# Optimization experiments

Measured on AMD Instinct MI355X. Metric: run time of the kernel, lower is better.

The kernel has to match this reference:

```python
import jax, jax.numpy as jnp
import numpy as np

N = 100_000   # nodes
E = 1_600_000 # edges
C = 64        # in = hidden = out channels
H = 8         # heads
D = C // H    # head_dim = 8
R = 4         # relations
L = 2         # layers


def setup_inputs() -> dict:
    key = jax.random.key(0)
    ks = jax.random.split(key, 10)
    sc = 1.0 / np.sqrt(C)  # xavier-ish scale
    return {
        "x": jax.random.normal(ks[0], (N, C), jnp.float32),
        "edge_index": jax.random.randint(ks[1], (2, E), 0, N),
        "edge_type": jax.random.randint(ks[2], (E,), 0, R),
        "W_Q": jax.random.normal(ks[3], (L, R, H, C, D), jnp.float32) * sc,
        "W_K": jax.random.normal(ks[4], (L, R, H, C, D), jnp.float32) * sc,
        "W_V": jax.random.normal(ks[5], (L, R, H, C, D), jnp.float32) * sc,
        "W_concat": jax.random.normal(ks[6], (L, R, H * D, C), jnp.float32) * sc,
        "sem_w": jax.random.normal(ks[7], (L, C), jnp.float32) * sc,
        "sem_b": jnp.zeros((L,), jnp.float32),
        "W_self": jax.random.normal(ks[8], (L, C, C), jnp.float32) * sc,
        "ln_g": jnp.ones((L, C), jnp.float32),
        "ln_b": jnp.zeros((L, C), jnp.float32),
    }


def _layer(x, src, dst, edge_type, WQ, WK, WV, Wcat, sw, sb, Ws, g, b):
    inv_sqrt_d = 1.0 / np.sqrt(D)
    rel_msgs = []
    for r in range(R):  # small fixed relation loop
        mask = (edge_type == r).astype(x.dtype)             # (E,)
        Q = jnp.einsum('nc,hcd->nhd', x, WQ[r])             # (N,H,D)
        K = jnp.einsum('nc,hcd->nhd', x, WK[r])
        V = jnp.einsum('nc,hcd->nhd', x, WV[r])
        # edge-wise QK energy, leaky_relu(0.01), scatter-add into dst node
        energy = jnp.einsum('ehd,ehd->eh', Q[dst], K[src]) * inv_sqrt_d
        energy = jax.nn.leaky_relu(energy)                  # (E,H)
        alpha_n = jax.ops.segment_sum(energy * mask[:, None], dst,
                                      num_segments=N)       # (N,H)
        alpha = jax.nn.softmax(alpha_n, axis=0)             # softmax over nodes
        w = alpha[dst] * mask[:, None]                      # (E,H)
        m = jax.ops.segment_sum(w[:, :, None] * V[src], dst,
                                num_segments=N)             # (N,H,D)
        rel_msgs.append(m.reshape(N, H * D) @ Wcat[r])      # (N,C)
    stacked = jnp.stack(rel_msgs)                           # (R,N,C)
    beta = jax.nn.softmax(stacked @ sw + sb, axis=0)        # (R,N) semantic attn
    agg = jnp.einsum('rn,rnc->nc', beta, stacked)           # (N,C)
    y = x + jax.nn.gelu(x @ Ws + agg, approximate=False)
    mu = y.mean(-1, keepdims=True)
    var = y.var(-1, keepdims=True)
    return (y - mu) / jnp.sqrt(var + 1e-5) * g + b


def reference(x, edge_index, edge_type, W_Q, W_K, W_V, W_concat,
              sem_w, sem_b, W_self, ln_g, ln_b):
    src, dst = edge_index[0], edge_index[1]  # PyG source_to_target: j=row0, i=row1
    for l in range(L):
        x = _layer(x, src, dst, edge_type, W_Q[l], W_K[l], W_V[l], W_concat[l],
                   sem_w[l], sem_b[l], W_self[l], ln_g[l], ln_b[l])
        # inter-layer dropout omitted (inference / eval mode)
    return x
```

## Files before the change

### kernel.cpp

```cpp
#include <hip/hip_runtime.h>
#include <hip/hip_bf16.h>

#define NN 100000
#define EE 1600000
#define RRR 4
#define HHH 8
#define NT 400000
#define GG 782
#define SHIFT 9
#define NBLK 512
#define CHUNK 3125
#define BMAX 2560

typedef unsigned int u32;
typedef unsigned short u16;
typedef __attribute__((ext_vector_type(8))) short bf16x8;
typedef __attribute__((ext_vector_type(4))) float f32x4;

static constexpr size_t OFF_KV   = 0;
static constexpr size_t OFF_Q    = 102400000;
static constexpr size_t OFF_S    = 153600000;
static constexpr size_t OFF_SELF = 204800000;
static constexpr size_t OFF_AL   = 217600000;
static constexpr size_t OFF_PW   = 230400000;
static constexpr size_t OFF_PART = 230700000;
static constexpr size_t OFF_FIN  = 230710000;
static constexpr size_t OFF_CW   = 230720000;
static constexpr size_t OFF_LG   = 230730000;
static constexpr size_t OFF_ROWP = 232400000;
static constexpr size_t OFF_EDG  = 234100000;
static constexpr size_t OFF_BSTORE = OFF_S;
static constexpr size_t OFF_HIST   = OFF_S + 8000000;
static constexpr size_t OFF_OFFA   = OFF_S + 16000000;
static constexpr size_t OFF_BASE   = OFF_S + 24000000;

__device__ inline u16 f2bf(float f){
  union { __hip_bfloat16 h; u16 u; } cv; cv.h = __float2bfloat16(f); return cv.u;
}
__device__ inline float bf2f(u16 u){ return __uint_as_float(((u32)u) << 16); }

__global__ __launch_bounds__(256) void k_histA(const int* __restrict__ dst, const int* __restrict__ typ,
                                               u32* __restrict__ Hist){
  __shared__ u32 h[GG];
  int b = blockIdx.x, t = threadIdx.x;
  for (int g = t; g < GG; g += 256) h[g] = 0u;
  __syncthreads();
  int e0 = b * CHUNK;
  for (int e = e0 + t; e < e0 + CHUNK; e += 256){
    int seg = typ[e] * NN + dst[e];
    atomicAdd(&h[seg >> SHIFT], 1u);
  }
  __syncthreads();
  for (int g = t; g < GG; g += 256) Hist[(size_t)b * GG + g] = h[g];
}

__global__ __launch_bounds__(1024) void k_base(const u32* __restrict__ Hist, u32* __restrict__ Base,
                                               u32* __restrict__ rowp){
  __shared__ u32 tot[GG];
  int t = threadIdx.x;
  if (t < GG){
    u32 s = 0;
    for (int b = 0; b < NBLK; b++) s += Hist[(size_t)b * GG + t];
    tot[t] = s;
  }
  __syncthreads();
  if (t == 0){
    u32 acc = 0;
    for (int g = 0; g < GG; g++){ u32 c = tot[g]; Base[g] = acc; acc += c; }
    Base[GG] = acc;
    rowp[NT] = EE;
  }
}

__global__ __launch_bounds__(512) void k_off(const u32* __restrict__ Hist, const u32* __restrict__ Base,
                                             u32* __restrict__ Off){
  __shared__ u32 v[NBLK];
  int g = blockIdx.x, t = threadIdx.x;
  v[t] = Hist[(size_t)t * GG + g];
  __syncthreads();
  if (t == 0){
    u32 acc = Base[g];
    for (int b = 0; b < NBLK; b++){ u32 c = v[b]; v[b] = acc; acc += c; }
  }
  __syncthreads();
  Off[(size_t)g * NBLK + t] = v[t];
}

__global__ __launch_bounds__(256) void k_fill(const int* __restrict__ src, const int* __restrict__ dst,
                                              const int* __restrict__ typ, const u32* __restrict__ Off,
                                              u32* __restrict__ bstore){
  __shared__ u32 cur[GG];
  int b = blockIdx.x, t = threadIdx.x;
  for (int g = t; g < GG; g += 256) cur[g] = Off[(size_t)g * NBLK + b];
  __syncthreads();
  int e0 = b * CHUNK;
  for (int e = e0 + t; e < e0 + CHUNK; e += 256){
    int seg = typ[e] * NN + dst[e];
    u32 pos = atomicAdd(&cur[seg >> SHIFT], 1u);
    bstore[pos] = ((u32)(seg & 511) << 17) | (u32)src[e];
  }
}

__global__ __launch_bounds__(256) void k_sortD(const u32* __restrict__ bstore, const u32* __restrict__ Base,
                                               u32* __restrict__ rowp, u32* __restrict__ edges){
  __shared__ u32 ent[BMAX];
  __shared__ u32 binc[512], bexc[512];
  int g = blockIdx.x, t = threadIdx.x;
  u32 base = Base[g];
  u32 cnt = Base[g + 1] - base;
  if (cnt > (u32)BMAX) cnt = (u32)BMAX;
  for (int i = t; i < 512; i += 256) binc[i] = 0u;
  __syncthreads();
  for (u32 i = t; i < cnt; i += 256){
    u32 v = bstore[base + i];
    ent[i] = v;
    atomicAdd(&binc[v >> 17], 1u);
  }
  __syncthreads();
  if (t == 0){
    u32 acc = 0;
    #pragma unroll 8
    for (int s = 0; s < 512; s++){ u32 c = binc[s]; bexc[s] = acc; binc[s] = acc; acc += c; }
  }
  __syncthreads();
  for (int s = t; s < 512; s += 256){
    int seg = g * 512 + s;
    if (seg < NT) rowp[seg] = base + bexc[s];
  }
  __syncthreads();
  for (u32 i = t; i < cnt; i += 256){
    u32 v = ent[i];
    u32 p = atomicAdd(&binc[v >> 17], 1u);
    edges[base + p] = v & 0x1FFFFu;
  }
}

__global__ __launch_bounds__(256) void k_repackbf(const float* __restrict__ WQ, const float* __restrict__ WK,
                                                  const float* __restrict__ WV, const float* __restrict__ Wcat,
                                                  const float* __restrict__ Wself, u16* __restrict__ pwB){
  int t = blockIdx.x * 256 + threadIdx.x;
  if (t >= 2 * 17 * 4096) return;
  int l = t / (17 * 4096), rem = t % (17 * 4096);
  int mat = rem >> 12, idx = rem & 4095;
  int out = idx >> 6, c = idx & 63;
  float v;
  if (mat < 12){
    int kind = mat >> 2, r = mat & 3;
    int h = out >> 3, d = out & 7;
    const float* Wsrc = (kind == 0) ? WQ : (kind == 1) ? WK : WV;
    v = Wsrc[((((l * RRR + r) * HHH + h) * 64) + c) * 8 + d];
  } else if (mat == 12){
    v = Wself[(l * 64 + c) * 64 + out];
  } else {
    int r = mat - 13;
    v = Wcat[(((l * RRR + r) * 64) + c) * 64 + out];
  }
  pwB[t] = f2bf(v);
}

__global__ __launch_bounds__(512) void k_cw(const float* __restrict__ Wcat, const float* __restrict__ semw,
                                            float* __restrict__ cw){
  int t = threadIdx.x;
  int l = t >> 8, r = (t >> 6) & 3, k = t & 63;
  const float* wp = Wcat + (((size_t)(l * RRR + r) * 64) + k) * 64;
  const float* sp = semw + l * 64;
  float s = 0.f;
  #pragma unroll 8
  for (int c = 0; c < 64; c++) s += wp[c] * sp[c];
  cw[t] = s;
}


__global__ __launch_bounds__(256) void k_qkvself(const float* __restrict__ x, const u16* __restrict__ pwL,
                                                 u16* __restrict__ QAll, u16* __restrict__ selfb,
                                                 u32* __restrict__ kvpAll){
  __shared__ u16 xa[64][72];
  int t = threadIdx.x;
  int n0 = blockIdx.x * 64;
  {
    int row = t >> 2, c0 = (t & 3) * 16;
    int n = n0 + row;
    float4 v0 = {}, v1 = {}, v2 = {}, v3 = {};
    if (n < NN){
      const float4* xp = (const float4*)(x + (size_t)n * 64 + c0);
      v0 = xp[0]; v1 = xp[1]; v2 = xp[2]; v3 = xp[3];
    }
    ushort4* dp = (ushort4*)&xa[row][c0];
    dp[0] = make_ushort4(f2bf(v0.x), f2bf(v0.y), f2bf(v0.z), f2bf(v0.w));
    dp[1] = make_ushort4(f2bf(v1.x), f2bf(v1.y), f2bf(v1.z), f2bf(v1.w));
    dp[2] = make_ushort4(f2bf(v2.x), f2bf(v2.y), f2bf(v2.z), f2bf(v2.w));
    dp[3] = make_ushort4(f2bf(v3.x), f2bf(v3.y), f2bf(v3.z), f2bf(v3.w));
  }
  __syncthreads();
  int w = t >> 6, lane = t & 63;
  int ra = w * 16 + (lane & 15);
  int kg = (lane >> 4) * 8;
  int cb = lane & 15;
  int rb = (lane >> 4) * 4;
  bf16x8 a0 = *(const bf16x8*)&xa[ra][kg];
  bf16x8 a1 = *(const bf16x8*)&xa[ra][32 + kg];
  f32x4 z = {0.f, 0.f, 0.f, 0.f};
  #pragma unroll
  for (int m = 0; m < 5; m++){
    const u16* wp = pwL + (size_t)((m < 4) ? m : 12) * 4096;
    f32x4 acc[4] = {z, z, z, z};
    #pragma unroll
    for (int t4 = 0; t4 < 4; t4++){
      bf16x8 b0 = *(const bf16x8*)(wp + (t4 * 16 + cb) * 64 + kg);
      bf16x8 b1 = *(const bf16x8*)(wp + (t4 * 16 + cb) * 64 + 32 + kg);
      acc[t4] = __builtin_amdgcn_mfma_f32_16x16x32_bf16(a0, b0, acc[t4], 0, 0, 0);
      acc[t4] = __builtin_amdgcn_mfma_f32_16x16x32_bf16(a1, b1, acc[t4], 0, 0, 0);
    }
    u16* op = (m < 4) ? (QAll + (size_t)m * NN * 64) : selfb;
    #pragma unroll
    for (int t4 = 0; t4 < 4; t4++){
      #pragma unroll
      for (int i2 = 0; i2 < 4; i2++){
        int n = n0 + w * 16 + rb + i2;
        if (n < NN) op[(size_t)n * 64 + t4 * 16 + cb] = f2bf(acc[t4][i2]);
      }
    }
  }
  #pragma unroll
  for (int r = 0; r < 4; r++){
    const u16* wk = pwL + (size_t)(4 + r) * 4096;
    const u16* wv = pwL + (size_t)(8 + r) * 4096;
    f32x4 ak[4] = {z, z, z, z};
    f32x4 av[4] = {z, z, z, z};
    #pragma unroll
    for (int t4 = 0; t4 < 4; t4++){
      bf16x8 bk0 = *(const bf16x8*)(wk + (t4 * 16 + cb) * 64 + kg);
      bf16x8 bk1 = *(const bf16x8*)(wk + (t4 * 16 + cb) * 64 + 32 + kg);
      bf16x8 bv0 = *(const bf16x8*)(wv + (t4 * 16 + cb) * 64 + kg);
      bf16x8 bv1 = *(const bf16x8*)(wv + (t4 * 16 + cb) * 64 + 32 + kg);
      ak[t4] = __builtin_amdgcn_mfma_f32_16x16x32_bf16(a0, bk0, ak[t4], 0, 0, 0);
      ak[t4] = __builtin_amdgcn_mfma_f32_16x16x32_bf16(a1, bk1, ak[t4], 0, 0, 0);
      av[t4] = __builtin_amdgcn_mfma_f32_16x16x32_bf16(a0, bv0, av[t4], 0, 0, 0);
      av[t4] = __builtin_amdgcn_mfma_f32_16x16x32_bf16(a1, bv1, av[t4], 0, 0, 0);
    }
    u32* kp = kvpAll + (size_t)r * NN * 64;
    #pragma unroll
    for (int t4 = 0; t4 < 4; t4++){
      #pragma unroll
      for (int i2 = 0; i2 < 4; i2++){
        int n = n0 + w * 16 + rb + i2;
        if (n < NN) kp[(size_t)n * 64 + t4 * 16 + cb] = (u32)f2bf(ak[t4][i2]) | ((u32)f2bf(av[t4][i2]) << 16);
      }
    }
  }
}

__global__ __launch_bounds__(256) void k_gather4(const u32* __restrict__ edges, const u32* __restrict__ rowp,
                                                 const u32* __restrict__ kvpAll, const u16* __restrict__ QAll,
                                                 u16* __restrict__ Sb, float* __restrict__ alphaB){
  int wid = threadIdx.x >> 6, lane = threadIdx.x & 63;
  int qt = lane >> 4;
  int i  = lane & 15;
  int n = blockIdx.x * 4 + wid;
  const float isd = 0.35355339059327373f;
  #pragma unroll
  for (int r = 0; r < 4; r++){
    const u32* kvp = kvpAll + (size_t)r * NN * 64;
    ushort4 qv = *(const ushort4*)&QAll[((size_t)r * NN + n) * 64 + 4 * i];
    float q0 = bf2f(qv.x), q1 = bf2f(qv.y), q2 = bf2f(qv.z), q3 = bf2f(qv.w);
    u32 beg = rowp[(size_t)r * NN + n], end = rowp[(size_t)r * NN + n + 1];
    float sx = 0.f, sy = 0.f, sz = 0.f, sw = 0.f, aa = 0.f;
    for (u32 base = beg; base < end; base += 64){
      u32 cnt = (end - base < 64u) ? (end - base) : 64u;
      u32 eidx = (base + (u32)lane < end) ? edges[base + lane] : 0u;
      for (u32 j = 0; j < cnt; j += 4){
        u32 jj = j + (u32)qt;
        float mk = (jj < cnt) ? 1.f : 0.f;
        u32 js = (jj < cnt) ? jj : (cnt - 1);
        int s = __shfl((int)eidx, (int)js);
        uint4 w = *(const uint4*)&kvp[(size_t)s * 64 + 4 * i];
        float p = q0 * bf2f((u16)(w.x & 0xFFFFu)) + q1 * bf2f((u16)(w.y & 0xFFFFu))
                + q2 * bf2f((u16)(w.z & 0xFFFFu)) + q3 * bf2f((u16)(w.w & 0xFFFFu));
        p += __shfl_xor(p, 1);
        float e = p * isd;
        e = (e > 0.f) ? e : 0.01f * e;
        aa += e * mk;
        sx += bf2f((u16)(w.x >> 16)) * mk;
        sy += bf2f((u16)(w.y >> 16)) * mk;
        sz += bf2f((u16)(w.z >> 16)) * mk;
        sw += bf2f((u16)(w.w >> 16)) * mk;
      }
    }
    sx += __shfl_xor(sx, 16); sx += __shfl_xor(sx, 32);
    sy += __shfl_xor(sy, 16); sy += __shfl_xor(sy, 32);
    sz += __shfl_xor(sz, 16); sz += __shfl_xor(sz, 32);
    sw += __shfl_xor(sw, 16); sw += __shfl_xor(sw, 32);
    aa += __shfl_xor(aa, 16); aa += __shfl_xor(aa, 32);
    if (qt == 0){
      ushort4 o; o.x = f2bf(sx); o.y = f2bf(sy); o.z = f2bf(sz); o.w = f2bf(sw);
      *(ushort4*)&Sb[((size_t)r * NN + n) * 64 + 4 * i] = o;
      if ((i & 1) == 0) alphaB[((size_t)r * NN + n) * 8 + (i >> 1)] = aa;
    }
  }
}

__global__ __launch_bounds__(256) void k_stats1(const float* __restrict__ alpha, float2* __restrict__ part){
  int r = blockIdx.y;
  int chunk = blockIdx.x;
  const int per = (NN + 31) / 32;
  int nbeg = chunk * per;
  int nend = nbeg + per; if (nend > NN) nend = NN;
  int t = threadIdx.x;
  int h = t & 7;
  int g = t >> 3;
  float m = -1e30f, s = 0.f;
  for (int n = nbeg + g; n < nend; n += 32){
    float a = alpha[((size_t)r * NN + n) * 8 + h];
    if (a > m){ s *= expf(m - a); m = a; }
    s += expf(a - m);
  }
  __shared__ float sm[256], ss[256];
  sm[t] = m; ss[t] = s; __syncthreads();
  for (int off = 128; off >= 8; off >>= 1){
    if (t < off){
      float m2 = sm[t + off], s2 = ss[t + off];
      float M = fmaxf(sm[t], m2);
      ss[t] = ss[t] * expf(sm[t] - M) + s2 * expf(m2 - M);
      sm[t] = M;
    }
    __syncthreads();
  }
  if (t < 8) part[(r * 8 + t) * 32 + chunk] = make_float2(sm[t], ss[t]);
}

__global__ void k_stats2(const float2* __restrict__ part, float2* __restrict__ fin){
  int col = threadIdx.x;
  if (col < 32){
    float M = -1e30f, S = 0.f;
    for (int i = 0; i < 32; i++){
      float2 p = part[col * 32 + i];
      float Mn = fmaxf(M, p.x);
      S = S * expf(M - Mn) + p.y * expf(p.x - Mn);
      M = Mn;
    }
    fin[col] = make_float2(M, 1.f / S);
  }
}

__global__ __launch_bounds__(256) void k_msg(const u16* __restrict__ S, const float* __restrict__ alpha,
                                             const float2* __restrict__ fin, const u16* __restrict__ pwCat,
                                             const float* __restrict__ cwL, float* __restrict__ lgbuf,
                                             u16* __restrict__ stacked){
  __shared__ u16 xa[64][72];
  __shared__ u16 wt[64][72];
  int r = blockIdx.y;
  int t = threadIdx.x;
  int n0 = blockIdx.x * 64;
  {
    int row = t >> 2, c0 = (t & 3) * 16;
    int n = n0 + row;
    int na = (n < NN) ? n : (NN - 1);
    int h0 = c0 >> 3;
    float2 f0 = fin[r * 8 + h0];
    float2 f1 = fin[r * 8 + h0 + 1];
    float a0 = alpha[((size_t)r * NN + na) * 8 + h0];
    float a1 = alpha[((size_t)r * NN + na) * 8 + h0 + 1];
    float w0 = expf(a0 - f0.x) * f0.y;
    float w1 = expf(a1 - f1.x) * f1.y;
    const u32* sp = (const u32*)(S + ((size_t)r * NN + na) * 64 + c0);
    const float* cwr = cwL + r * 64;
    float lgp = 0.f;
    #pragma unroll
    for (int jj = 0; jj < 8; jj++){
      u32 bts = sp[jj];
      float wm = (jj < 4) ? w0 : w1;
      float mv0 = bf2f((u16)(bts & 0xFFFFu)) * wm;
      float mv1 = bf2f((u16)(bts >> 16)) * wm;
      lgp += mv0 * cwr[c0 + jj * 2] + mv1 * cwr[c0 + jj * 2 + 1];
      ushort2 o;
      o.x = f2bf(mv0);
      o.y = f2bf(mv1);
      *(ushort2*)&xa[row][c0 + jj * 2] = o;
    }
    lgp += __shfl_xor(lgp, 1);
    lgp += __shfl_xor(lgp, 2);
    if ((t & 3) == 0 && n < NN) lgbuf[(size_t)r * NN + n] = lgp;
  }
  {
    const u32* p0 = (const u32*)(pwCat + (size_t)r * 4096);
    for (int idx = t; idx < 2048; idx += 256){
      int out = idx >> 5, cc = idx & 31;
      *(u32*)&wt[out][cc * 2] = p0[idx];
    }
  }
  __syncthreads();
  int w = t >> 6, lane = t & 63;
  int ra = w * 16 + (lane & 15);
  int kg = (lane >> 4) * 8;
  int cb = lane & 15;
  int rb = (lane >> 4) * 4;
  bf16x8 a0 = *(const bf16x8*)&xa[ra][kg];
  bf16x8 a1 = *(const bf16x8*)&xa[ra][32 + kg];
  f32x4 z = {0.f, 0.f, 0.f, 0.f};
  f32x4 acc[4] = {z, z, z, z};
  #pragma unroll
  for (int t4 = 0; t4 < 4; t4++){
    bf16x8 b0 = *(const bf16x8*)&wt[t4 * 16 + cb][kg];
    bf16x8 b1 = *(const bf16x8*)&wt[t4 * 16 + cb][32 + kg];
    acc[t4] = __builtin_amdgcn_mfma_f32_16x16x32_bf16(a0, b0, acc[t4], 0, 0, 0);
    acc[t4] = __builtin_amdgcn_mfma_f32_16x16x32_bf16(a1, b1, acc[t4], 0, 0, 0);
  }
  #pragma unroll
  for (int t4 = 0; t4 < 4; t4++){
    #pragma unroll
    for (int i = 0; i < 4; i++){
      int n = n0 + w * 16 + rb + i;
      if (n < NN) stacked[((size_t)r * NN + n) * 64 + t4 * 16 + cb] = f2bf(acc[t4][i]);
    }
  }
}

__global__ __launch_bounds__(256) void k_final(const u16* __restrict__ stacked, const u16* __restrict__ selfb,
                                               const float* __restrict__ xin, const float* __restrict__ lgbuf,
                                               const float* __restrict__ lng, const float* __restrict__ lnb,
                                               float* __restrict__ xout){
  int t = threadIdx.x;
  int wid = t >> 6, lane = t & 63;
  int n = blockIdx.x * 4 + wid;
  float st[4];
  #pragma unroll
  for (int r = 0; r < 4; r++) st[r] = bf2f(stacked[((size_t)r * NN + n) * 64 + lane]);
  float lg0 = lgbuf[n];
  float lg1 = lgbuf[(size_t)NN + n];
  float lg2 = lgbuf[(size_t)2 * NN + n];
  float lg3 = lgbuf[(size_t)3 * NN + n];
  float mx = fmaxf(fmaxf(lg0, lg1), fmaxf(lg2, lg3));
  float e0 = expf(lg0 - mx), e1 = expf(lg1 - mx), e2 = expf(lg2 - mx), e3 = expf(lg3 - mx);
  float inv = 1.f / (e0 + e1 + e2 + e3);
  float agg = (e0 * st[0] + e1 * st[1] + e2 * st[2] + e3 * st[3]) * inv;
  float pre = bf2f(selfb[(size_t)n * 64 + lane]) + agg;
  float ge = 0.5f * pre * (1.f + erff(pre * 0.70710678118654752f));
  float y = xin[(size_t)n * 64 + lane] + ge;
  float mu = y;
  #pragma unroll
  for (int o = 1; o < 64; o <<= 1) mu += __shfl_xor(mu, o);
  mu *= (1.f / 64.f);
  float d = y - mu;
  float vv = d * d;
  #pragma unroll
  for (int o = 1; o < 64; o <<= 1) vv += __shfl_xor(vv, o);
  vv *= (1.f / 64.f);
  xout[(size_t)n * 64 + lane] = d * rsqrtf(vv + 1e-5f) * lng[lane] + lnb[lane];
}

extern "C" void kernel_launch(void* const* d_in, const int* in_sizes, int n_in,
                              void* d_out, int out_size, void* d_ws, size_t ws_size,
                              hipStream_t stream){
  const float* x0    = (const float*)d_in[0];
  const int*   eidx  = (const int*)d_in[1];
  const int*   etyp  = (const int*)d_in[2];
  const float* WQ    = (const float*)d_in[3];
  const float* WK    = (const float*)d_in[4];
  const float* WV    = (const float*)d_in[5];
  const float* Wcat  = (const float*)d_in[6];
  const float* semw  = (const float*)d_in[7];
  const float* semb  = (const float*)d_in[8];
  const float* Wself = (const float*)d_in[9];
  const float* lng   = (const float*)d_in[10];
  const float* lnb   = (const float*)d_in[11];
  float* out = (float*)d_out;
  char* ws = (char*)d_ws;

  const int* srcArr = eidx;
  const int* dstArr = eidx + EE;

  u32*  kvpAll   = (u32*)(ws + OFF_KV);
  u16*  Qb       = (u16*)(ws + OFF_Q);
  u16*  stackedB = (u16*)(ws + OFF_Q);
  u16*  Sb       = (u16*)(ws + OFF_S);
  u16*  selfb    = (u16*)(ws + OFF_SELF);
  float* alphaB  = (float*)(ws + OFF_AL);
  u16*  pwB      = (u16*)(ws + OFF_PW);
  float2* part   = (float2*)(ws + OFF_PART);
  float2* fin    = (float2*)(ws + OFF_FIN);
  float* cw      = (float*)(ws + OFF_CW);
  float* lgbuf   = (float*)(ws + OFF_LG);
  u32* rowp   = (u32*)(ws + OFF_ROWP);
  u32* edges  = (u32*)(ws + OFF_EDG);
  u32* bstore = (u32*)(ws + OFF_BSTORE);
  u32* Hist   = (u32*)(ws + OFF_HIST);
  u32* Off    = (u32*)(ws + OFF_OFFA);
  u32* Base   = (u32*)(ws + OFF_BASE);

  k_histA<<<NBLK, 256, 0, stream>>>(dstArr, etyp, Hist);
  k_base<<<1, 1024, 0, stream>>>(Hist, Base, rowp);
  k_off<<<GG, 512, 0, stream>>>(Hist, Base, Off);
  k_fill<<<NBLK, 256, 0, stream>>>(srcArr, dstArr, etyp, Off, bstore);
  k_sortD<<<GG, 256, 0, stream>>>(bstore, Base, rowp, edges);
  k_repackbf<<<(2 * 17 * 4096 + 255) / 256, 256, 0, stream>>>(WQ, WK, WV, Wcat, Wself, pwB);
  k_cw<<<1, 512, 0, stream>>>(Wcat, semw, cw);

  for (int l = 0; l < 2; l++){
    const float* xcur = (l == 0) ? x0 : out;
    const u16* pwL = pwB + (size_t)l * 17 * 4096;
    k_qkvself<<<1563, 256, 0, stream>>>(xcur, pwL, Qb, selfb, kvpAll);
    k_gather4<<<NN / 4, 256, 0, stream>>>(edges, rowp, kvpAll, Qb, Sb, alphaB);
    k_stats1<<<dim3(32, 4), 256, 0, stream>>>(alphaB, part);
    k_stats2<<<1, 64, 0, stream>>>(part, fin);
    k_msg<<<dim3(1563, 4), 256, 0, stream>>>(Sb, alphaB, fin, pwL + (size_t)13 * 4096,
                                             cw + l * 256, lgbuf, stackedB);
    k_final<<<NN / 4, 256, 0, stream>>>(stackedB, selfb, xcur, lgbuf,
                                        lng + l * 64, lnb + l * 64, out);
  }
  (void)in_sizes; (void)n_in; (void)out_size; (void)ws_size;
  (void)semb;
}
```

Measured before the change: 725.2 us.

## Fuse message projection, semantic attention, self-GEMM and LayerNorm into one kernel

Merges k_msg (per-relation Wcat projection) and k_final (semantic softmax, GELU, residual, LayerNorm) into one kernel that handles all four relations per 64-node tile. The semantic weights are computed in shared memory and applied to the MFMA results in registers. The x@W_self GEMM moves out of k_qkvself into the fused kernel. This avoids writing and re-reading the bf16 stacked buffer, selfb and lgbuf and removes one launch per layer. The cost is much larger shared memory per block (about 46KB), which may lower occupancy, and Wcat is now read from global memory instead of staged in LDS.

```diff
diff --git a/kernel.cpp b/kernel.cpp
--- a/kernel.cpp
+++ b/kernel.cpp
@@ -20,13 +20,11 @@
 static constexpr size_t OFF_KV   = 0;
 static constexpr size_t OFF_Q    = 102400000;
 static constexpr size_t OFF_S    = 153600000;
-static constexpr size_t OFF_SELF = 204800000;
 static constexpr size_t OFF_AL   = 217600000;
 static constexpr size_t OFF_PW   = 230400000;
 static constexpr size_t OFF_PART = 230700000;
 static constexpr size_t OFF_FIN  = 230710000;
 static constexpr size_t OFF_CW   = 230720000;
-static constexpr size_t OFF_LG   = 230730000;
 static constexpr size_t OFF_ROWP = 232400000;
 static constexpr size_t OFF_EDG  = 234100000;
 static constexpr size_t OFF_BSTORE = OFF_S;
@@ -172,8 +170,7 @@
 
 
 __global__ __launch_bounds__(256) void k_qkvself(const float* __restrict__ x, const u16* __restrict__ pwL,
-                                                 u16* __restrict__ QAll, u16* __restrict__ selfb,
-                                                 u32* __restrict__ kvpAll){
+                                                 u16* __restrict__ QAll, u32* __restrict__ kvpAll){
   __shared__ u16 xa[64][72];
   int t = threadIdx.x;
   int n0 = blockIdx.x * 64;
@@ -201,8 +198,8 @@
   bf16x8 a1 = *(const bf16x8*)&xa[ra][32 + kg];
   f32x4 z = {0.f, 0.f, 0.f, 0.f};
   #pragma unroll
-  for (int m = 0; m < 5; m++){
-    const u16* wp = pwL + (size_t)((m < 4) ? m : 12) * 4096;
+  for (int m = 0; m < 4; m++){
+    const u16* wp = pwL + (size_t)m * 4096;
     f32x4 acc[4] = {z, z, z, z};
     #pragma unroll
     for (int t4 = 0; t4 < 4; t4++){
@@ -211,7 +208,7 @@
       acc[t4] = __builtin_amdgcn_mfma_f32_16x16x32_bf16(a0, b0, acc[t4], 0, 0, 0);
       acc[t4] = __builtin_amdgcn_mfma_f32_16x16x32_bf16(a1, b1, acc[t4], 0, 0, 0);
     }
-    u16* op = (m < 4) ? (QAll + (size_t)m * NN * 64) : selfb;
+    u16* op = QAll + (size_t)m * NN * 64;
     #pragma unroll
     for (int t4 = 0; t4 < 4; t4++){
       #pragma unroll
@@ -342,16 +339,33 @@
   }
 }
 
-__global__ __launch_bounds__(256) void k_msg(const u16* __restrict__ S, const float* __restrict__ alpha,
-                                             const float2* __restrict__ fin, const u16* __restrict__ pwCat,
-                                             const float* __restrict__ cwL, float* __restrict__ lgbuf,
-                                             u16* __restrict__ stacked){
+__global__ __launch_bounds__(256) void k_msgfin(const u16* __restrict__ S, const float* __restrict__ alpha,
+                                                const float2* __restrict__ fin, const u16* __restrict__ pwL,
+                                                const float* __restrict__ cwL, const float* __restrict__ xin,
+                                                const float* __restrict__ lng, const float* __restrict__ lnb,
+                                                float* __restrict__ xout){
+  __shared__ u16 As[4][64][72];
   __shared__ u16 xa[64][72];
-  __shared__ u16 wt[64][72];
-  int r = blockIdx.y;
+  __shared__ float lgs[4][64];
+  __shared__ float beta[4][64];
   int t = threadIdx.x;
   int n0 = blockIdx.x * 64;
   {
+    int row = t >> 2, c0 = (t & 3) * 16;
+    int n = n0 + row;
+    float4 v0 = {}, v1 = {}, v2 = {}, v3 = {};
+    if (n < NN){
+      const float4* xp = (const float4*)(xin + (size_t)n * 64 + c0);
+      v0 = xp[0]; v1 = xp[1]; v2 = xp[2]; v3 = xp[3];
+    }
+    ushort4* dp = (ushort4*)&xa[row][c0];
+    dp[0] = make_ushort4(f2bf(v0.x), f2bf(v0.y), f2bf(v0.z), f2bf(v0.w));
+    dp[1] = make_ushort4(f2bf(v1.x), f2bf(v1.y), f2bf(v1.z), f2bf(v1.w));
+    dp[2] = make_ushort4(f2bf(v2.x), f2bf(v2.y), f2bf(v2.z), f2bf(v2.w));
+    dp[3] = make_ushort4(f2bf(v3.x), f2bf(v3.y), f2bf(v3.z), f2bf(v3.w));
+  }
+  #pragma unroll
+  for (int r = 0; r < 4; r++){
     int row = t >> 2, c0 = (t & 3) * 16;
     int n = n0 + row;
     int na = (n < NN) ? n : (NN - 1);
@@ -375,18 +389,19 @@
       ushort2 o;
       o.x = f2bf(mv0);
       o.y = f2bf(mv1);
-      *(ushort2*)&xa[row][c0 + jj * 2] = o;
+      *(ushort2*)&As[r][row][c0 + jj * 2] = o;
     }
     lgp += __shfl_xor(lgp, 1);
     lgp += __shfl_xor(lgp, 2);
-    if ((t & 3) == 0 && n < NN) lgbuf[(size_t)r * NN + n] = lgp;
-  }
-  {
-    const u32* p0 = (const u32*)(pwCat + (size_t)r * 4096);
-    for (int idx = t; idx < 2048; idx += 256){
-      int out = idx >> 5, cc = idx & 31;
-      *(u32*)&wt[out][cc * 2] = p0[idx];
-    }
+    if ((t & 3) == 0) lgs[r][row] = lgp;
+  }
+  __syncthreads();
+  if (t < 64){
+    float l0 = lgs[0][t], l1 = lgs[1][t], l2 = lgs[2][t], l3 = lgs[3][t];
+    float mx = fmaxf(fmaxf(l0, l1), fmaxf(l2, l3));
+    float e0 = expf(l0 - mx), e1 = expf(l1 - mx), e2 = expf(l2 - mx), e3 = expf(l3 - mx);
+    float inv = 1.f / (e0 + e1 + e2 + e3);
+    beta[0][t] = e0 * inv; beta[1][t] = e1 * inv; beta[2][t] = e2 * inv; beta[3][t] = e3 * inv;
   }
   __syncthreads();
   int w = t >> 6, lane = t & 63;
@@ -394,58 +409,78 @@
   int kg = (lane >> 4) * 8;
   int cb = lane & 15;
   int rb = (lane >> 4) * 4;
-  bf16x8 a0 = *(const bf16x8*)&xa[ra][kg];
-  bf16x8 a1 = *(const bf16x8*)&xa[ra][32 + kg];
   f32x4 z = {0.f, 0.f, 0.f, 0.f};
-  f32x4 acc[4] = {z, z, z, z};
+  f32x4 agg[4] = {z, z, z, z};
+  #pragma unroll
+  for (int r = 0; r < 4; r++){
+    bf16x8 a0 = *(const bf16x8*)&As[r][ra][kg];
+    bf16x8 a1 = *(const bf16x8*)&As[r][ra][32 + kg];
+    const u16* wp = pwL + (size_t)(13 + r) * 4096;
+    float br[4];
+    #pragma unroll
+    for (int i2 = 0; i2 < 4; i2++) br[i2] = beta[r][w * 16 + rb + i2];
+    #pragma unroll
+    for (int t4 = 0; t4 < 4; t4++){
+      f32x4 acc = z;
+      bf16x8 b0 = *(const bf16x8*)(wp + (t4 * 16 + cb) * 64 + kg);
+      bf16x8 b1 = *(const bf16x8*)(wp + (t4 * 16 + cb) * 64 + 32 + kg);
+      acc = __builtin_amdgcn_mfma_f32_16x16x32_bf16(a0, b0, acc, 0, 0, 0);
+      acc = __builtin_amdgcn_mfma_f32_16x16x32_bf16(a1, b1, acc, 0, 0, 0);
+      #pragma unroll
+      for (int i2 = 0; i2 < 4; i2++) agg[t4][i2] += br[i2] * acc[i2];
+    }
+  }
+  {
+    bf16x8 a0 = *(const bf16x8*)&xa[ra][kg];
+    bf16x8 a1 = *(const bf16x8*)&xa[ra][32 + kg];
+    const u16* wp = pwL + (size_t)12 * 4096;
+    #pragma unroll
+    for (int t4 = 0; t4 < 4; t4++){
+      f32x4 acc = z;
+      bf16x8 b0 = *(const bf16x8*)(wp + (t4 * 16 + cb) * 64 + kg);
+      bf16x8 b1 = *(const bf16x8*)(wp + (t4 * 16 + cb) * 64 + 32 + kg);
+      acc = __builtin_amdgcn_mfma_f32_16x16x32_bf16(a0, b0, acc, 0, 0, 0);
+      acc = __builtin_amdgcn_mfma_f32_16x16x32_bf16(a1, b1, acc, 0, 0, 0);
+      agg[t4] += acc;
+    }
+  }
+  float ys[4][4];
   #pragma unroll
   for (int t4 = 0; t4 < 4; t4++){
-    bf16x8 b0 = *(const bf16x8*)&wt[t4 * 16 + cb][kg];
-    bf16x8 b1 = *(const bf16x8*)&wt[t4 * 16 + cb][32 + kg];
-    acc[t4] = __builtin_amdgcn_mfma_f32_16x16x32_bf16(a0, b0, acc[t4], 0, 0, 0);
-    acc[t4] = __builtin_amdgcn_mfma_f32_16x16x32_bf16(a1, b1, acc[t4], 0, 0, 0);
+    #pragma unroll
+    for (int i2 = 0; i2 < 4; i2++){
+      int n = n0 + w * 16 + rb + i2;
+      int ch = t4 * 16 + cb;
+      float pre = agg[t4][i2];
+      float ge = 0.5f * pre * (1.f + erff(pre * 0.70710678118654752f));
+      float xv = (n < NN) ? xin[(size_t)n * 64 + ch] : 0.f;
+      ys[t4][i2] = xv + ge;
+    }
+  }
+  float mu[4], rs[4];
+  #pragma unroll
+  for (int i2 = 0; i2 < 4; i2++){
+    float s = (ys[0][i2] + ys[1][i2]) + (ys[2][i2] + ys[3][i2]);
+    s += __shfl_xor(s, 1); s += __shfl_xor(s, 2); s += __shfl_xor(s, 4); s += __shfl_xor(s, 8);
+    mu[i2] = s * (1.f / 64.f);
+  }
+  #pragma unroll
+  for (int i2 = 0; i2 < 4; i2++){
+    float d0 = ys[0][i2] - mu[i2], d1 = ys[1][i2] - mu[i2];
+    float d2 = ys[2][i2] - mu[i2], d3 = ys[3][i2] - mu[i2];
+    float v = (d0 * d0 + d1 * d1) + (d2 * d2 + d3 * d3);
+    v += __shfl_xor(v, 1); v += __shfl_xor(v, 2); v += __shfl_xor(v, 4); v += __shfl_xor(v, 8);
+    rs[i2] = rsqrtf(v * (1.f / 64.f) + 1e-5f);
   }
   #pragma unroll
   for (int t4 = 0; t4 < 4; t4++){
     #pragma unroll
-    for (int i = 0; i < 4; i++){
-      int n = n0 + w * 16 + rb + i;
-      if (n < NN) stacked[((size_t)r * NN + n) * 64 + t4 * 16 + cb] = f2bf(acc[t4][i]);
-    }
-  }
-}
-
-__global__ __launch_bounds__(256) void k_final(const u16* __restrict__ stacked, const u16* __restrict__ selfb,
-                                               const float* __restrict__ xin, const float* __restrict__ lgbuf,
-                                               const float* __restrict__ lng, const float* __restrict__ lnb,
-                                               float* __restrict__ xout){
-  int t = threadIdx.x;
-  int wid = t >> 6, lane = t & 63;
-  int n = blockIdx.x * 4 + wid;
-  float st[4];
-  #pragma unroll
-  for (int r = 0; r < 4; r++) st[r] = bf2f(stacked[((size_t)r * NN + n) * 64 + lane]);
-  float lg0 = lgbuf[n];
-  float lg1 = lgbuf[(size_t)NN + n];
-  float lg2 = lgbuf[(size_t)2 * NN + n];
-  float lg3 = lgbuf[(size_t)3 * NN + n];
-  float mx = fmaxf(fmaxf(lg0, lg1), fmaxf(lg2, lg3));
-  float e0 = expf(lg0 - mx), e1 = expf(lg1 - mx), e2 = expf(lg2 - mx), e3 = expf(lg3 - mx);
-  float inv = 1.f / (e0 + e1 + e2 + e3);
-  float agg = (e0 * st[0] + e1 * st[1] + e2 * st[2] + e3 * st[3]) * inv;
-  float pre = bf2f(selfb[(size_t)n * 64 + lane]) + agg;
-  float ge = 0.5f * pre * (1.f + erff(pre * 0.70710678118654752f));
-  float y = xin[(size_t)n * 64 + lane] + ge;
-  float mu = y;
-  #pragma unroll
-  for (int o = 1; o < 64; o <<= 1) mu += __shfl_xor(mu, o);
-  mu *= (1.f / 64.f);
-  float d = y - mu;
-  float vv = d * d;
-  #pragma unroll
-  for (int o = 1; o < 64; o <<= 1) vv += __shfl_xor(vv, o);
-  vv *= (1.f / 64.f);
-  xout[(size_t)n * 64 + lane] = d * rsqrtf(vv + 1e-5f) * lng[lane] + lnb[lane];
+    for (int i2 = 0; i2 < 4; i2++){
+      int n = n0 + w * 16 + rb + i2;
+      int ch = t4 * 16 + cb;
+      if (n < NN) xout[(size_t)n * 64 + ch] = (ys[t4][i2] - mu[i2]) * rs[i2] * lng[ch] + lnb[ch];
+    }
+  }
 }
 
 extern "C" void kernel_launch(void* const* d_in, const int* in_sizes, int n_in,
@@ -471,15 +506,12 @@
 
   u32*  kvpAll   = (u32*)(ws + OFF_KV);
   u16*  Qb       = (u16*)(ws + OFF_Q);
-  u16*  stackedB = (u16*)(ws + OFF_Q);
   u16*  Sb       = (u16*)(ws + OFF_S);
-  u16*  selfb    = (u16*)(ws + OFF_SELF);
   float* alphaB  = (float*)(ws + OFF_AL);
   u16*  pwB      = (u16*)(ws + OFF_PW);
   float2* part   = (float2*)(ws + OFF_PART);
   float2* fin    = (float2*)(ws + OFF_FIN);
   float* cw      = (float*)(ws + OFF_CW);
-  float* lgbuf   = (float*)(ws + OFF_LG);
   u32* rowp   = (u32*)(ws + OFF_ROWP);
   u32* edges  = (u32*)(ws + OFF_EDG);
   u32* bstore = (u32*)(ws + OFF_BSTORE);
@@ -498,14 +530,12 @@
   for (int l = 0; l < 2; l++){
     const float* xcur = (l == 0) ? x0 : out;
     const u16* pwL = pwB + (size_t)l * 17 * 4096;
-    k_qkvself<<<1563, 256, 0, stream>>>(xcur, pwL, Qb, selfb, kvpAll);
+    k_qkvself<<<1563, 256, 0, stream>>>(xcur, pwL, Qb, kvpAll);
     k_gather4<<<NN / 4, 256, 0, stream>>>(edges, rowp, kvpAll, Qb, Sb, alphaB);
     k_stats1<<<dim3(32, 4), 256, 0, stream>>>(alphaB, part);
     k_stats2<<<1, 64, 0, stream>>>(part, fin);
-    k_msg<<<dim3(1563, 4), 256, 0, stream>>>(Sb, alphaB, fin, pwL + (size_t)13 * 4096,
-                                             cw + l * 256, lgbuf, stackedB);
-    k_final<<<NN / 4, 256, 0, stream>>>(stackedB, selfb, xcur, lgbuf,
-                                        lng + l * 64, lnb + l * 64, out);
+    k_msgfin<<<1563, 256, 0, stream>>>(Sb, alphaB, fin, pwL, cw + l * 256, xcur,
+                                       lng + l * 64, lnb + l * 64, out);
   }
   (void)in_sizes; (void)n_in; (void)out_size; (void)ws_size;
   (void)semb;
```

Result: no change. 722.1 us (-0.4%).
